# Optimization experiments

Hardware: AMD Instinct MI355X
Metric: run time of the kernel (lower is better)

## Reference

```python
import jax, jax.numpy as jnp
import numpy as np

STRIDES = (8, 16, 32, 64, 128)
HS = (192, 96, 48, 24, 12)
NUM_CLASSES = 15
NUM_THETA = 18
B = 16
SCORE_THR = 0.05
IOU_THR = 0.3
MAX_DET = 1000


def setup_inputs() -> dict:
    key = jax.random.key(0)
    ks = jax.random.split(key, 20)
    inp = {}
    i = 0
    for name, c in (("cls", NUM_CLASSES), ("reg", 5), ("tc", NUM_THETA), ("tr", 1)):
        for l, h in enumerate(HS):
            inp[f"{name}_l{l}"] = jax.random.normal(ks[i], (B, c, h, h), dtype=jnp.float32)
            i += 1
    return inp


def _coords():
    # FCOS-style location centers per level, concatenated: [N, 2] (x, y)
    outs = []
    for h, s in zip(HS, STRIDES):
        c1d = jnp.arange(h, dtype=jnp.float32) * s + s // 2
        yy, xx = jnp.meshgrid(c1d, c1d, indexing="ij")
        outs.append(jnp.stack([xx.ravel(), yy.ravel()], axis=-1))
    return jnp.concatenate(outs, axis=0)


def _flatten(levels):
    # list of [B,C,h,w] -> [B, sum(h*w), C]  (permute to NHWC then reshape, as in torch)
    b = levels[0].shape[0]
    return jnp.concatenate(
        [jnp.transpose(t, (0, 2, 3, 1)).reshape(b, -1, t.shape[1]) for t in levels], axis=1
    )


def _pairwise_iou(boxes):
    # boxes [M,5] (x1,y1,x2,y2,theta); axis-aligned IoU on first 4 coords
    x1, y1, x2, y2 = boxes[:, 0], boxes[:, 1], boxes[:, 2], boxes[:, 3]
    area = jnp.clip(x2 - x1, 0.0) * jnp.clip(y2 - y1, 0.0)
    iw = jnp.clip(jnp.minimum(x2[:, None], x2[None, :]) - jnp.maximum(x1[:, None], x1[None, :]), 0.0)
    ih = jnp.clip(jnp.minimum(y2[:, None], y2[None, :]) - jnp.maximum(y1[:, None], y1[None, :]), 0.0)
    inter = iw * ih
    union = area[:, None] + area[None, :] - inter
    return inter / jnp.maximum(union, 1e-8)


def _nms_keep(boxes, valid, iou_thr):
    # greedy NMS over score-sorted boxes; returns bool keep mask [M]
    m = boxes.shape[0]
    iou = _pairwise_iou(boxes)
    idx = jnp.arange(m)

    def body(i, keep):
        sup = keep[i] & (iou[i] > iou_thr) & (idx > i)
        return keep & ~sup

    return jax.lax.fori_loop(0, m, body, valid)


def _forward(cls_levels, reg_levels, tc_levels, tr_levels):
    coords = _coords()  # [N,2]

    cls_preds = jax.nn.sigmoid(_flatten(cls_levels))          # [B,N,15]
    cls_scores = jnp.max(cls_preds, axis=-1)                   # [B,N]
    cls_classes = jnp.argmax(cls_preds, axis=-1) + 1           # [B,N]

    tc_preds = jax.nn.sigmoid(_flatten(tc_levels))             # [B,N,18]
    theta_c = (jnp.argmax(tc_preds, axis=-1) + 1)[..., None].astype(jnp.float32)  # [B,N,1]
    tr_lo = _flatten(tr_levels)                                # [B,N,1]
    theta = theta_c * 10.0 + tr_lo                             # [B,N,1]

    # reg: scale ltrb channels (0:4) by stride per level, keep angle channel raw
    reg_parts = []
    for t, s in zip(reg_levels, STRIDES):
        r = jnp.transpose(t, (0, 2, 3, 1)).reshape(t.shape[0], -1, 5)
        reg_parts.append(jnp.concatenate([r[..., :4] * float(s), r[..., 4:]], axis=-1))
    reg = jnp.concatenate(reg_parts, axis=1)                   # [B,N,5]

    x1y1 = coords[None, :, :] - reg[..., :2]
    x2y2 = coords[None, :, :] + reg[..., 2:4]
    boxes = jnp.concatenate([x1y1, x2y2, theta], axis=-1)      # [B,N,5]

    max_num = min(MAX_DET, cls_scores.shape[-1])
    top_scores, top_idx = jax.lax.top_k(cls_scores, max_num)   # sorted desc
    boxes_topk = jnp.take_along_axis(boxes, top_idx[..., None], axis=1)   # [B,M,5]
    classes_topk = jnp.take_along_axis(cls_classes, top_idx, axis=1)      # [B,M]

    valid = top_scores >= SCORE_THR
    keep = jax.vmap(lambda b, v: _nms_keep(b, v, IOU_THR))(boxes_topk, valid)  # [B,M] bool

    scores_post = top_scores * keep
    classes_post = classes_topk * keep
    boxes_post = boxes_topk * keep[..., None]
    return scores_post, classes_post, boxes_post


def reference(cls_l0, cls_l1, cls_l2, cls_l3, cls_l4,
              reg_l0, reg_l1, reg_l2, reg_l3, reg_l4,
              tc_l0, tc_l1, tc_l2, tc_l3, tc_l4,
              tr_l0, tr_l1, tr_l2, tr_l3, tr_l4):
    return _forward(
        [cls_l0, cls_l1, cls_l2, cls_l3, cls_l4],
        [reg_l0, reg_l1, reg_l2, reg_l3, reg_l4],
        [tc_l0, tc_l1, tc_l2, tc_l3, tc_l4],
        [tr_l0, tr_l1, tr_l2, tr_l3, tr_l4],
    )
```

## Files before the change

### kernel.cpp

```cpp
#include <hip/hip_runtime.h>
#include <stdint.h>

#define NCLS   15
#define NTH    18
#define BATCH  16
#define NANCH  49104
#define KTOP   1000
#define NWORDS 16
#define NBIN   32768
#define BSHIFT 15
#define CAND   2048

__device__ __forceinline__ float sigmoidf(float x) {
    return 1.0f / (1.0f + expf(-x));
}

__device__ __forceinline__ void levelOf(int i, int& lvl, int& h, int& s, int& pos) {
    if (i < 36864)      { lvl = 0; h = 192; s = 8;   pos = i; }
    else if (i < 46080) { lvl = 1; h = 96;  s = 16;  pos = i - 36864; }
    else if (i < 48384) { lvl = 2; h = 48;  s = 32;  pos = i - 46080; }
    else if (i < 48960) { lvl = 3; h = 24;  s = 64;  pos = i - 48384; }
    else                { lvl = 4; h = 12;  s = 128; pos = i - 48960; }
}

__device__ __forceinline__ unsigned long long shfl_u64(unsigned long long v, int src) {
    int lo = __shfl((int)(unsigned int)(v & 0xFFFFFFFFull), src);
    int hi = __shfl((int)(unsigned int)(v >> 32), src);
    return ((unsigned long long)(unsigned int)hi << 32) | (unsigned long long)(unsigned int)lo;
}

__device__ __forceinline__ void atomicOr64Shared(unsigned long long* p, unsigned long long v) {
    unsigned int* q = (unsigned int*)p;
    unsigned int lo = (unsigned int)v;
    unsigned int hi = (unsigned int)(v >> 32);
    if (lo) atomicOr(q, lo);
    if (hi) atomicOr(q + 1, hi);
}

__global__ __launch_bounds__(256) void k_scores(
    const float* __restrict__ c0, const float* __restrict__ c1,
    const float* __restrict__ c2, const float* __restrict__ c3,
    const float* __restrict__ c4,
    float* __restrict__ scores, unsigned char* __restrict__ classes)
{
    int g4 = blockIdx.x * 256 + threadIdx.x;
    if (g4 >= BATCH * NANCH / 4) return;
    int g = g4 * 4;
    int b = g / NANCH;
    int i = g - b * NANCH;
    int lvl, h, s, pos;
    levelOf(i, lvl, h, s, pos);
    int hh = h * h;
    const float* cp = (lvl == 0) ? c0 : (lvl == 1) ? c1 : (lvl == 2) ? c2
                      : (lvl == 3) ? c3 : c4;
    const float* base = cp + (size_t)b * NCLS * hh + pos;
    float4 best = make_float4(-1e30f, -1e30f, -1e30f, -1e30f);
    int bcx = 0, bcy = 0, bcz = 0, bcw = 0;
    #pragma unroll
    for (int c = 0; c < NCLS; ++c) {
        float4 v = *(const float4*)(base + (size_t)c * hh);
        float sx = sigmoidf(v.x), sy = sigmoidf(v.y);
        float sz = sigmoidf(v.z), sw = sigmoidf(v.w);
        if (sx > best.x) { best.x = sx; bcx = c; }
        if (sy > best.y) { best.y = sy; bcy = c; }
        if (sz > best.z) { best.z = sz; bcz = c; }
        if (sw > best.w) { best.w = sw; bcw = c; }
    }
    *(float4*)(scores + g) = best;
    *(uchar4*)(classes + g) = make_uchar4(
        (unsigned char)(bcx + 1), (unsigned char)(bcy + 1),
        (unsigned char)(bcz + 1), (unsigned char)(bcw + 1));
}

__global__ __launch_bounds__(1024) void k_histT(
    const float* __restrict__ scores, int* __restrict__ tbin, int* __restrict__ tcnt)
{
    const int b   = blockIdx.x;
    const int tid = threadIdx.x;
    __shared__ unsigned int lh[NBIN / 2];
    __shared__ unsigned int csum[1024];
    __shared__ int s_c, s_T;

    for (int i = tid; i < NBIN / 2; i += 1024) lh[i] = 0u;
    if (tid == 0) { s_c = 0; s_T = 0; tcnt[b * 16] = 0; }
    __syncthreads();

    const float4* sv = (const float4*)(scores + (size_t)b * NANCH);
    for (int f4 = tid; f4 < NANCH / 4; f4 += 1024) {
        float4 v = sv[f4];
        unsigned int bin;
        bin = __float_as_uint(v.x) >> BSHIFT;
        atomicAdd(&lh[bin >> 1], 1u << ((bin & 1) << 4));
        bin = __float_as_uint(v.y) >> BSHIFT;
        atomicAdd(&lh[bin >> 1], 1u << ((bin & 1) << 4));
        bin = __float_as_uint(v.z) >> BSHIFT;
        atomicAdd(&lh[bin >> 1], 1u << ((bin & 1) << 4));
        bin = __float_as_uint(v.w) >> BSHIFT;
        atomicAdd(&lh[bin >> 1], 1u << ((bin & 1) << 4));
    }
    __syncthreads();

    unsigned int s = 0;
    #pragma unroll
    for (int k = 0; k < 16; ++k) {
        unsigned int w = lh[tid * 16 + k];
        s += (w & 0xFFFFu) + (w >> 16);
    }
    csum[tid] = s;
    __syncthreads();
    for (int d = 1; d < 1024; d <<= 1) {
        unsigned int add = (tid + d < 1024) ? csum[tid + d] : 0u;
        __syncthreads();
        csum[tid] += add;
        __syncthreads();
    }
    if (csum[tid] >= (unsigned)KTOP &&
        (tid == 1023 || csum[tid + 1] < (unsigned)KTOP))
        s_c = tid;
    __syncthreads();
    const int c = s_c;
    const unsigned int hi = (c < 1023) ? csum[c + 1] : 0u;

    if (tid < 64) {
        unsigned int cnt = 0;
        if (tid < 32) {
            int bin = c * 32 + tid;
            cnt = (lh[bin >> 1] >> ((bin & 1) << 4)) & 0xFFFFu;
        }
        unsigned int suf = cnt;
        #pragma unroll
        for (int d = 1; d < 32; d <<= 1) {
            unsigned int o = __shfl_down(suf, d);
            if (tid + d < 32) suf += o;
        }
        unsigned int nxt = __shfl_down(suf, 1);
        if (tid < 32) {
            if (hi + suf >= (unsigned)KTOP &&
                (tid == 31 || hi + nxt < (unsigned)KTOP))
                s_T = c * 32 + tid;
        }
    }
    __syncthreads();
    if (tid == 0) tbin[b] = s_T;
}

__global__ __launch_bounds__(256) void k_compact(
    const float* __restrict__ scores, const int* __restrict__ tbin,
    int* __restrict__ cnt, unsigned long long* __restrict__ cand)
{
    const int b = blockIdx.y;
    const int t4 = blockIdx.x * 256 + threadIdx.x;
    __shared__ int lcnt;
    __shared__ int lbase;
    if (threadIdx.x == 0) lcnt = 0;
    __syncthreads();

    const int T = tbin[b];
    const bool in = (t4 < NANCH / 4);
    float4 v = make_float4(0.f, 0.f, 0.f, 0.f);
    if (in) v = *(const float4*)(scores + (size_t)b * NANCH + 4 * (size_t)t4);
    unsigned int bits[4] = { __float_as_uint(v.x), __float_as_uint(v.y),
                             __float_as_uint(v.z), __float_as_uint(v.w) };
    int rank[4];
    #pragma unroll
    for (int k = 0; k < 4; ++k) {
        bool pass = in && ((int)(bits[k] >> BSHIFT) >= T);
        rank[k] = pass ? atomicAdd(&lcnt, 1) : -1;
    }
    __syncthreads();
    if (threadIdx.x == 0) lbase = atomicAdd(&cnt[b * 16], lcnt);
    __syncthreads();
    const int base = lbase;
    #pragma unroll
    for (int k = 0; k < 4; ++k) {
        if (rank[k] >= 0) {
            int p = base + rank[k];
            if (p < CAND) {
                unsigned int idx = 4u * (unsigned int)t4 + (unsigned int)k;
                cand[(size_t)b * CAND + p] =
                    ((unsigned long long)bits[k] << 32) |
                    (unsigned long long)(0xFFFFFFFFu - idx);
            }
        }
    }
}

__global__ __launch_bounds__(256) void k_rankdec(
    const unsigned long long* __restrict__ cand, const int* __restrict__ cnt,
    const float* __restrict__ r0, const float* __restrict__ r1,
    const float* __restrict__ r2, const float* __restrict__ r3,
    const float* __restrict__ r4,
    const unsigned char* __restrict__ classes_all,
    float* __restrict__ tsc, int* __restrict__ tix,
    float* __restrict__ boxes, int* __restrict__ clstop)
{
    const int b  = blockIdx.y;
    const int ci = blockIdx.x * 256 + threadIdx.x;
    __shared__ unsigned long long keys[CAND];

    int n = cnt[b * 16]; if (n > CAND) n = CAND;
    for (int i = threadIdx.x; i < CAND; i += 256)
        keys[i] = (i < n) ? cand[(size_t)b * CAND + i] : 0ull;
    __syncthreads();

    const unsigned long long my = keys[ci];
    if (my == 0ull) return;

    int rank = 0;
    #pragma unroll 8
    for (int j = 0; j < CAND; ++j)
        rank += (keys[j] > my) ? 1 : 0;
    if (rank >= KTOP) return;

    const int g   = b * KTOP + rank;
    const int idx = (int)(0xFFFFFFFFu - (unsigned int)(my & 0xFFFFFFFFull));
    tsc[g] = __uint_as_float((unsigned int)(my >> 32));
    tix[g] = idx;
    clstop[g] = (int)classes_all[(size_t)b * NANCH + idx];

    int lvl, h, s, pos;
    levelOf(idx, lvl, h, s, pos);
    int y = pos / h, x = pos - y * h;
    int hh = h * h;
    const float* rp = (lvl == 0) ? r0 : (lvl == 1) ? r1 : (lvl == 2) ? r2
                      : (lvl == 3) ? r3 : r4;
    const float* rb = rp + (size_t)b * 5 * hh + pos;
    float fs = (float)s;
    float rr0 = rb[0] * fs;
    float rr1 = rb[(size_t)hh] * fs;
    float rr2 = rb[(size_t)2 * hh] * fs;
    float rr3 = rb[(size_t)3 * hh] * fs;
    float cx = (float)(x * s + (s >> 1));
    float cy = (float)(y * s + (s >> 1));
    float* op = boxes + (size_t)g * 5;
    op[0] = cx - rr0;
    op[1] = cy - rr1;
    op[2] = cx + rr2;
    op[3] = cy + rr3;
}

__global__ __launch_bounds__(256) void k_masktheta(
    const float* __restrict__ boxes_in, unsigned long long* __restrict__ mask,
    const float* __restrict__ t0, const float* __restrict__ t1,
    const float* __restrict__ t2, const float* __restrict__ t3,
    const float* __restrict__ t4,
    const float* __restrict__ q0, const float* __restrict__ q1,
    const float* __restrict__ q2, const float* __restrict__ q3,
    const float* __restrict__ q4,
    const int* __restrict__ tix, float* __restrict__ boxes_theta)
{
    const int b = blockIdx.x;
    const int role = blockIdx.y;

    if (role < 16) {
        const int by = role;
        __shared__ float bx1[1024], by1[1024], bx2[1024], by2[1024], bar[1024];
        for (int r = threadIdx.x; r < 1024; r += 256) {
            float x1 = 0.f, y1 = 0.f, x2 = 0.f, y2 = 0.f;
            if (r < KTOP) {
                const float* p = boxes_in + ((size_t)(b * KTOP + r)) * 5;
                x1 = p[0]; y1 = p[1]; x2 = p[2]; y2 = p[3];
            }
            bx1[r] = x1; by1[r] = y1; bx2[r] = x2; by2[r] = y2;
            bar[r] = fmaxf(x2 - x1, 0.0f) * fmaxf(y2 - y1, 0.0f);
        }
        __syncthreads();

        const int l  = threadIdx.x & 63;
        const int wv = threadIdx.x >> 6;
        const int i  = (by << 6) + l;
        const float x1 = bx1[i], y1 = by1[i], x2 = bx2[i], y2 = by2[i], ai = bar[i];

        for (int w = by + wv; w < NWORDS; w += 4) {
            const int j0 = w << 6;
            unsigned long long m = 0ull;
            #pragma unroll 8
            for (int jj = 0; jj < 64; ++jj) {
                const int j = j0 + jj;
                float iw = fminf(x2, bx2[j]) - fmaxf(x1, bx1[j]);
                iw = fmaxf(iw, 0.0f);
                float ih = fminf(y2, by2[j]) - fmaxf(y1, by1[j]);
                ih = fmaxf(ih, 0.0f);
                float inter = iw * ih;
                float u = ai + bar[j] - inter;
                float iou = inter / fmaxf(u, 1e-8f);
                unsigned long long bit = (iou > 0.3f && j > i) ? 1ull : 0ull;
                m |= bit << jj;
            }
            mask[(((size_t)b * 1024 + i) << 4) + w] = m;
        }
    } else {
        int r = (role - 16) * 4 + (threadIdx.x >> 6);
        if (r >= KTOP) return;
        int lane = threadIdx.x & 63;
        int wid = b * KTOP + r;
        int idx = tix[wid];

        int lvl, h, s, pos;
        levelOf(idx, lvl, h, s, pos);
        int hh = h * h;
        const float* tp = (lvl == 0) ? t0 : (lvl == 1) ? t1 : (lvl == 2) ? t2
                          : (lvl == 3) ? t3 : t4;
        const float* qp = (lvl == 0) ? q0 : (lvl == 1) ? q1 : (lvl == 2) ? q2
                          : (lvl == 3) ? q3 : q4;

        float v = -1e30f;
        if (lane < NTH)
            v = sigmoidf(tp[(size_t)b * NTH * hh + pos + (size_t)lane * hh]);
        float m = v;
        m = fmaxf(m, __shfl_xor(m, 1));
        m = fmaxf(m, __shfl_xor(m, 2));
        m = fmaxf(m, __shfl_xor(m, 4));
        m = fmaxf(m, __shfl_xor(m, 8));
        m = fmaxf(m, __shfl_xor(m, 16));
        m = fmaxf(m, __shfl_xor(m, 32));
        unsigned long long eq = __ballot(v == m);
        int bt = __builtin_ctzll(eq);
        float tr = qp[(size_t)b * hh + pos];
        if (lane == 0)
            boxes_theta[(size_t)wid * 5 + 4] = (float)(bt + 1) * 10.0f + tr;
    }
}

#define LOADROW(R, W) do {                                                          \
    const ulonglong2* rp2 = (const ulonglong2*)(mask +                              \
        (((size_t)b * 1024 + ((W) << 6) + l) << 4));                                \
    _Pragma("unroll")                                                               \
    for (int p = 0; p < 8; ++p) {                                                   \
        ulonglong2 v = rp2[p]; R[2 * p] = v.x; R[2 * p + 1] = v.y;                  \
    }                                                                               \
} while (0)

#define PROC(W, R) do {                                                             \
    const unsigned long long rowword = R[W];                                        \
    unsigned long long zr = __ballot(rowword == 0ull);                              \
    unsigned long long remw = sremv[W];                                             \
    unsigned long long pend = vw[W] & ~remw;                                        \
    unsigned long long keptm = 0ull;                                                \
    while (pend) {                                                                  \
        unsigned long long nzp = pend & ~zr;                                        \
        if (!nzp) { keptm |= pend; break; }                                         \
        int jj = __builtin_ctzll(nzp);                                              \
        unsigned long long low = (1ull << jj); low = (low << 1) - 1ull;             \
        keptm |= pend & low;                                                        \
        remw |= shfl_u64(rowword, jj);                                              \
        pend &= ~low; pend &= ~remw;                                                \
    }                                                                               \
    if (l == 0) skeep[W] = keptm;                                                   \
    if ((keptm >> l) & 1ull) {                                                      \
        _Pragma("unroll")                                                           \
        for (int w2 = (W) + 1; w2 < NWORDS; ++w2)                                   \
            if (R[w2]) atomicOr64Shared(&sremv[w2], R[w2]);                         \
    }                                                                               \
} while (0)

__global__ __launch_bounds__(64) void k_nms(
    const unsigned long long* __restrict__ mask,
    const float* __restrict__ tsc, const int* __restrict__ clstop,
    const float* __restrict__ boxes, float* __restrict__ out)
{
    const int b = blockIdx.x;
    const int l = threadIdx.x;
    __shared__ unsigned long long sremv[NWORDS];
    __shared__ unsigned long long skeep[NWORDS];

    if (l < NWORDS) sremv[l] = 0ull;

    unsigned long long vw[NWORDS];
    #pragma unroll
    for (int w = 0; w < NWORDS; ++w) {
        int i = (w << 6) + l;
        bool v = (i < KTOP) && (tsc[b * KTOP + i] >= 0.05f);
        vw[w] = __ballot(v);
    }

    unsigned long long rowA[NWORDS], rowB[NWORDS];
    LOADROW(rowA, 0);
    LOADROW(rowB, 1);   PROC(0, rowA);
    LOADROW(rowA, 2);   PROC(1, rowB);
    LOADROW(rowB, 3);   PROC(2, rowA);
    LOADROW(rowA, 4);   PROC(3, rowB);
    LOADROW(rowB, 5);   PROC(4, rowA);
    LOADROW(rowA, 6);   PROC(5, rowB);
    LOADROW(rowB, 7);   PROC(6, rowA);
    LOADROW(rowA, 8);   PROC(7, rowB);
    LOADROW(rowB, 9);   PROC(8, rowA);
    LOADROW(rowA, 10);  PROC(9, rowB);
    LOADROW(rowB, 11);  PROC(10, rowA);
    LOADROW(rowA, 12);  PROC(11, rowB);
    LOADROW(rowB, 13);  PROC(12, rowA);
    LOADROW(rowA, 14);  PROC(13, rowB);
    LOADROW(rowB, 15);  PROC(14, rowA);
    PROC(15, rowB);

    #pragma unroll
    for (int w = 0; w < NWORDS; ++w) {
        int i = (w << 6) + l;
        if (i < KTOP) {
            int g = b * KTOP + i;
            float fk = (float)((skeep[w] >> l) & 1ull);
            out[g] = tsc[g] * fk;
            out[BATCH * KTOP + g] = (float)clstop[g] * fk;
            const float* bp = boxes + (size_t)g * 5;
            float* op = out + 2 * BATCH * KTOP + (size_t)g * 5;
            op[0] = bp[0] * fk;
            op[1] = bp[1] * fk;
            op[2] = bp[2] * fk;
            op[3] = bp[3] * fk;
            op[4] = bp[4] * fk;
        }
    }
}

extern "C" void kernel_launch(void* const* d_in, const int* in_sizes, int n_in,
                              void* d_out, int out_size, void* d_ws, size_t ws_size,
                              hipStream_t stream) {
    const float* c0 = (const float*)d_in[0];
    const float* c1 = (const float*)d_in[1];
    const float* c2 = (const float*)d_in[2];
    const float* c3 = (const float*)d_in[3];
    const float* c4 = (const float*)d_in[4];
    const float* r0 = (const float*)d_in[5];
    const float* r1 = (const float*)d_in[6];
    const float* r2 = (const float*)d_in[7];
    const float* r3 = (const float*)d_in[8];
    const float* r4 = (const float*)d_in[9];
    const float* t0 = (const float*)d_in[10];
    const float* t1 = (const float*)d_in[11];
    const float* t2 = (const float*)d_in[12];
    const float* t3 = (const float*)d_in[13];
    const float* t4 = (const float*)d_in[14];
    const float* q0 = (const float*)d_in[15];
    const float* q1 = (const float*)d_in[16];
    const float* q2 = (const float*)d_in[17];
    const float* q3 = (const float*)d_in[18];
    const float* q4 = (const float*)d_in[19];

    char* ws = (char*)d_ws;
    float*              scores  = (float*)(ws + 0);
    unsigned char*      classes = (unsigned char*)(ws + 3142656);
    int*                tcnt    = (int*)(ws + 3928320);
    int*                tbin    = (int*)(ws + 3929344);
    unsigned long long* cand    = (unsigned long long*)(ws + 3929408);
    float*              tsc     = (float*)(ws + 4191552);
    int*                tix     = (int*)(ws + 4255552);
    int*                clstop  = (int*)(ws + 4319552);
    float*              boxes   = (float*)(ws + 4383552);
    unsigned long long* mask    = (unsigned long long*)(ws + 4703552);
    float*              out     = (float*)d_out;

    k_scores<<<(BATCH * NANCH / 4 + 255) / 256, 256, 0, stream>>>(
        c0, c1, c2, c3, c4, scores, classes);
    k_histT<<<BATCH, 1024, 0, stream>>>(scores, tbin, tcnt);
    k_compact<<<dim3(48, BATCH), 256, 0, stream>>>(scores, tbin, tcnt, cand);
    k_rankdec<<<dim3(8, BATCH), 256, 0, stream>>>(
        cand, tcnt, r0, r1, r2, r3, r4, classes, tsc, tix, boxes, clstop);
    k_masktheta<<<dim3(BATCH, 16 + (KTOP + 3) / 4), 256, 0, stream>>>(
        boxes, mask, t0, t1, t2, t3, t4, q0, q1, q2, q3, q4, tix, boxes);
    k_nms<<<BATCH, 64, 0, stream>>>(mask, tsc, clstop, boxes, out);
}
```

Before: 104.7 us.

## Fuse histogram threshold and candidate compaction; drop shared staging in rank

Merges the histogram/threshold kernel and the compaction kernel into a single per-batch kernel, so the threshold stays in shared memory and one launch plus a global round trip goes away. The histogram is split into two shared copies chosen by thread index bit, meant to cut atomic contention. The rank kernel now reads candidates straight from global memory and loops only up to the real count instead of staging a fixed 2048 entries in shared memory. The trade-off is that compaction now runs on only 16 blocks with a single shared atomic counter, and the rank loop depends on cached global loads.

```diff
diff --git a/kernel.cpp b/kernel.cpp
--- a/kernel.cpp
+++ b/kernel.cpp
@@ -72,19 +72,22 @@
         (unsigned char)(bcz + 1), (unsigned char)(bcw + 1));
 }
 
-__global__ __launch_bounds__(1024) void k_histT(
-    const float* __restrict__ scores, int* __restrict__ tbin, int* __restrict__ tcnt)
+__global__ __launch_bounds__(1024) void k_histTC(
+    const float* __restrict__ scores,
+    int* __restrict__ cnt, unsigned long long* __restrict__ cand)
 {
     const int b   = blockIdx.x;
     const int tid = threadIdx.x;
-    __shared__ unsigned int lh[NBIN / 2];
+    __shared__ unsigned int lhA[NBIN / 2];
+    __shared__ unsigned int lhB[NBIN / 2];
     __shared__ unsigned int csum[1024];
-    __shared__ int s_c, s_T;
-
-    for (int i = tid; i < NBIN / 2; i += 1024) lh[i] = 0u;
-    if (tid == 0) { s_c = 0; s_T = 0; tcnt[b * 16] = 0; }
-    __syncthreads();
-
+    __shared__ int s_c, s_T, s_cnt;
+
+    for (int i = tid; i < NBIN / 2; i += 1024) { lhA[i] = 0u; lhB[i] = 0u; }
+    if (tid == 0) { s_c = 0; s_T = 0; s_cnt = 0; }
+    __syncthreads();
+
+    unsigned int* lh = (tid & 64) ? lhB : lhA;
     const float4* sv = (const float4*)(scores + (size_t)b * NANCH);
     for (int f4 = tid; f4 < NANCH / 4; f4 += 1024) {
         float4 v = sv[f4];
@@ -103,8 +106,9 @@
     unsigned int s = 0;
     #pragma unroll
     for (int k = 0; k < 16; ++k) {
-        unsigned int w = lh[tid * 16 + k];
-        s += (w & 0xFFFFu) + (w >> 16);
+        unsigned int wA = lhA[tid * 16 + k];
+        unsigned int wB = lhB[tid * 16 + k];
+        s += (wA & 0xFFFFu) + (wA >> 16) + (wB & 0xFFFFu) + (wB >> 16);
     }
     csum[tid] = s;
     __syncthreads();
@@ -122,12 +126,13 @@
     const unsigned int hi = (c < 1023) ? csum[c + 1] : 0u;
 
     if (tid < 64) {
-        unsigned int cnt = 0;
+        unsigned int bc = 0;
         if (tid < 32) {
             int bin = c * 32 + tid;
-            cnt = (lh[bin >> 1] >> ((bin & 1) << 4)) & 0xFFFFu;
-        }
-        unsigned int suf = cnt;
+            int sh = (bin & 1) << 4;
+            bc = ((lhA[bin >> 1] >> sh) & 0xFFFFu) + ((lhB[bin >> 1] >> sh) & 0xFFFFu);
+        }
+        unsigned int suf = bc;
         #pragma unroll
         for (int d = 1; d < 32; d <<= 1) {
             unsigned int o = __shfl_down(suf, d);
@@ -141,48 +146,27 @@
         }
     }
     __syncthreads();
-    if (tid == 0) tbin[b] = s_T;
-}
-
-__global__ __launch_bounds__(256) void k_compact(
-    const float* __restrict__ scores, const int* __restrict__ tbin,
-    int* __restrict__ cnt, unsigned long long* __restrict__ cand)
-{
-    const int b = blockIdx.y;
-    const int t4 = blockIdx.x * 256 + threadIdx.x;
-    __shared__ int lcnt;
-    __shared__ int lbase;
-    if (threadIdx.x == 0) lcnt = 0;
-    __syncthreads();
-
-    const int T = tbin[b];
-    const bool in = (t4 < NANCH / 4);
-    float4 v = make_float4(0.f, 0.f, 0.f, 0.f);
-    if (in) v = *(const float4*)(scores + (size_t)b * NANCH + 4 * (size_t)t4);
-    unsigned int bits[4] = { __float_as_uint(v.x), __float_as_uint(v.y),
-                             __float_as_uint(v.z), __float_as_uint(v.w) };
-    int rank[4];
-    #pragma unroll
-    for (int k = 0; k < 4; ++k) {
-        bool pass = in && ((int)(bits[k] >> BSHIFT) >= T);
-        rank[k] = pass ? atomicAdd(&lcnt, 1) : -1;
-    }
-    __syncthreads();
-    if (threadIdx.x == 0) lbase = atomicAdd(&cnt[b * 16], lcnt);
-    __syncthreads();
-    const int base = lbase;
-    #pragma unroll
-    for (int k = 0; k < 4; ++k) {
-        if (rank[k] >= 0) {
-            int p = base + rank[k];
-            if (p < CAND) {
-                unsigned int idx = 4u * (unsigned int)t4 + (unsigned int)k;
-                cand[(size_t)b * CAND + p] =
-                    ((unsigned long long)bits[k] << 32) |
-                    (unsigned long long)(0xFFFFFFFFu - idx);
+    const int T = s_T;
+
+    for (int f4 = tid; f4 < NANCH / 4; f4 += 1024) {
+        float4 v = sv[f4];
+        unsigned int bits[4] = { __float_as_uint(v.x), __float_as_uint(v.y),
+                                 __float_as_uint(v.z), __float_as_uint(v.w) };
+        #pragma unroll
+        for (int k = 0; k < 4; ++k) {
+            if ((int)(bits[k] >> BSHIFT) >= T) {
+                int p = atomicAdd(&s_cnt, 1);
+                if (p < CAND) {
+                    unsigned int idx = 4u * (unsigned int)f4 + (unsigned int)k;
+                    cand[(size_t)b * CAND + p] =
+                        ((unsigned long long)bits[k] << 32) |
+                        (unsigned long long)(0xFFFFFFFFu - idx);
+                }
             }
         }
     }
+    __syncthreads();
+    if (tid == 0) cnt[b * 16] = s_cnt;
 }
 
 __global__ __launch_bounds__(256) void k_rankdec(
@@ -196,20 +180,16 @@
 {
     const int b  = blockIdx.y;
     const int ci = blockIdx.x * 256 + threadIdx.x;
-    __shared__ unsigned long long keys[CAND];
-
     int n = cnt[b * 16]; if (n > CAND) n = CAND;
-    for (int i = threadIdx.x; i < CAND; i += 256)
-        keys[i] = (i < n) ? cand[(size_t)b * CAND + i] : 0ull;
-    __syncthreads();
-
-    const unsigned long long my = keys[ci];
-    if (my == 0ull) return;
+    if (ci >= n) return;
+
+    const unsigned long long* cb = cand + (size_t)b * CAND;
+    const unsigned long long my = cb[ci];
 
     int rank = 0;
-    #pragma unroll 8
-    for (int j = 0; j < CAND; ++j)
-        rank += (keys[j] > my) ? 1 : 0;
+    #pragma unroll 4
+    for (int j = 0; j < n; ++j)
+        rank += (cb[j] > my) ? 1 : 0;
     if (rank >= KTOP) return;
 
     const int g   = b * KTOP + rank;
@@ -440,19 +420,17 @@
     float*              scores  = (float*)(ws + 0);
     unsigned char*      classes = (unsigned char*)(ws + 3142656);
     int*                tcnt    = (int*)(ws + 3928320);
-    int*                tbin    = (int*)(ws + 3929344);
-    unsigned long long* cand    = (unsigned long long*)(ws + 3929408);
-    float*              tsc     = (float*)(ws + 4191552);
-    int*                tix     = (int*)(ws + 4255552);
-    int*                clstop  = (int*)(ws + 4319552);
-    float*              boxes   = (float*)(ws + 4383552);
-    unsigned long long* mask    = (unsigned long long*)(ws + 4703552);
+    unsigned long long* cand    = (unsigned long long*)(ws + 3929344);
+    float*              tsc     = (float*)(ws + 4191488);
+    int*                tix     = (int*)(ws + 4255488);
+    int*                clstop  = (int*)(ws + 4319488);
+    float*              boxes   = (float*)(ws + 4383488);
+    unsigned long long* mask    = (unsigned long long*)(ws + 4703488);
     float*              out     = (float*)d_out;
 
     k_scores<<<(BATCH * NANCH / 4 + 255) / 256, 256, 0, stream>>>(
         c0, c1, c2, c3, c4, scores, classes);
-    k_histT<<<BATCH, 1024, 0, stream>>>(scores, tbin, tcnt);
-    k_compact<<<dim3(48, BATCH), 256, 0, stream>>>(scores, tbin, tcnt, cand);
+    k_histTC<<<BATCH, 1024, 0, stream>>>(scores, tcnt, cand);
     k_rankdec<<<dim3(8, BATCH), 256, 0, stream>>>(
         cand, tcnt, r0, r1, r2, r3, r4, classes, tsc, tix, boxes, clstop);
     k_masktheta<<<dim3(BATCH, 16 + (KTOP + 3) / 4), 256, 0, stream>>>(
```

Result: slower. 124.6 us (+19.0%).
